# Optimization experiments

Measured on AMD Instinct MI355X. Metric: run time of the kernel, lower is better.

Reference implementation:

```python
import jax, jax.numpy as jnp
import numpy as np
from jax.scipy.special import logsumexp

# Complete binary tree, heap indexing: node i has children 2i+1, 2i+2.
# Edge for child c (c >= 1) is edge_pot[c-1], shape [C, C]:
#   rows = parent state, cols = child state (matches torch code's
#   logsumexp(edge + msg, dim=1) upward and edge.T downward).
DEPTH = 18
C = 16
N = 2 ** (DEPTH + 1) - 1  # 524287 nodes, N-1 edges


def setup_inputs() -> dict:
    key = jax.random.key(0)
    k1, k2 = jax.random.split(key)
    unary = jax.random.normal(k1, (N, C), dtype=jnp.float32)
    edge_pot = jax.random.normal(k2, (N - 1, C, C), dtype=jnp.float32)
    return {"unary": unary, "edge_pot": edge_pot, "depth": DEPTH}


def reference(unary, edge_pot, depth):
    """Sum-product belief propagation on a complete binary tree.

    Returns beliefs [N, C]: for each node v,
      belief[v] = unary[v] + sum(up messages from children) + down message from parent,
    identical to the per-message torch BFS loop, but processed level-parallel.
    """
    c = unary.shape[1]
    # ---------- upward pass (leaves -> root) ----------
    # subtotal[v] = unary[v] + sum of up-messages from v's children (V2F to parent factor)
    subtotal = unary
    m_up = jnp.zeros_like(unary)  # m_up[ch] = F2V message from edge (parent, ch) to parent
    for d in range(depth, 0, -1):
        lo, hi = 2 ** d - 1, 2 ** (d + 1) - 1          # children level, size 2^d
        ep = edge_pot[lo - 1:hi - 1]                    # [2^d, C, C]
        # logsumexp over child state (axis 2): torch's logsumexp(edge + msg, dim=1)
        msg = logsumexp(ep + subtotal[lo:hi][:, None, :], axis=2)  # [2^d, C]
        m_up = m_up.at[lo:hi].set(msg)
        plo, phi = 2 ** (d - 1) - 1, 2 ** d - 1
        # children of consecutive parents are consecutive pairs (2p+1, 2p+2)
        subtotal = subtotal.at[plo:phi].add(msg.reshape(-1, 2, c).sum(axis=1))
    # ---------- downward pass (root -> leaves) ----------
    m_down = jnp.zeros_like(unary)  # m_down[ch] = F2V message from edge (parent, ch) to ch
    for d in range(1, depth + 1):
        lo, hi = 2 ** d - 1, 2 ** (d + 1) - 1
        plo, phi = 2 ** (d - 1) - 1, 2 ** d - 1
        # V2F from parent p towards child ch: all incoming F2V at p except m_up[ch]
        par_total = jnp.repeat(subtotal[plo:phi] + m_down[plo:phi], 2, axis=0)  # [2^d, C]
        v2f = par_total - m_up[lo:hi]
        ep_t = jnp.swapaxes(edge_pot[lo - 1:hi - 1], 1, 2)  # edge.T: [2^d, Cchild, Cparent]
        msg = logsumexp(ep_t + v2f[:, None, :], axis=2)     # logsumexp over parent state
        m_down = m_down.at[lo:hi].set(msg)
    return subtotal + m_down  # beliefs [N, C]
```

## Files before the change

kernel.cpp:

```cpp
#include <hip/hip_runtime.h>
#include <stdint.h>


#ifndef __has_builtin
#define __has_builtin(x) 0
#endif
#if __has_builtin(__builtin_amdgcn_cvt_pk_fp8_f32) && __has_builtin(__builtin_amdgcn_cvt_f32_fp8)
#define EP8_FP8 1
#define EPC_BYTES 256
#else
#define EP8_FP8 0
#define EPC_BYTES 512
#endif

__device__ __forceinline__ void ldvec16(const float* p, float* d) {
    const float4* q = (const float4*)p;
    #pragma unroll
    for (int t = 0; t < 4; ++t) {
        float4 a = q[t];
        d[4*t+0] = a.x; d[4*t+1] = a.y; d[4*t+2] = a.z; d[4*t+3] = a.w;
    }
}

__device__ __forceinline__ float lse16_rs(const float* r, const float* s) {
    float v[16];
    float m;
    #pragma unroll
    for (int j = 0; j < 16; ++j) {
        v[j] = r[j] + s[j];
        m = (j == 0) ? v[0] : fmaxf(m, v[j]);
    }
    float acc = 0.f;
    #pragma unroll
    for (int j = 0; j < 16; ++j) acc += __expf(v[j] - m);
    return m + __logf(acc);
}

__device__ __forceinline__ void enc_row(uint8_t* dst, const float* r) {
#if EP8_FP8
    int w[4];
    #pragma unroll
    for (int t = 0; t < 4; ++t) {
        int x = __builtin_amdgcn_cvt_pk_fp8_f32(r[4*t+0], r[4*t+1], 0, false);
        x     = __builtin_amdgcn_cvt_pk_fp8_f32(r[4*t+2], r[4*t+3], x, true);
        w[t] = x;
    }
    *(int4*)dst = make_int4(w[0], w[1], w[2], w[3]);
#else
    uint32_t w[8];
    #pragma unroll
    for (int t = 0; t < 8; ++t) {
        uint32_t lo = __float_as_uint(r[2*t+0]);
        uint32_t hi = __float_as_uint(r[2*t+1]);
        w[t] = (lo >> 16) | (hi & 0xffff0000u);
    }
    ((int4*)dst)[0] = make_int4(w[0], w[1], w[2], w[3]);
    ((int4*)dst)[1] = make_int4(w[4], w[5], w[6], w[7]);
#endif
}

__device__ __forceinline__ void dec_row(const uint8_t* src, float* r) {
#if EP8_FP8
    uint4 w = *(const uint4*)src;
    uint32_t ws[4] = {w.x, w.y, w.z, w.w};
    #pragma unroll
    for (int t = 0; t < 4; ++t) {
        uint32_t u = ws[t];
        r[4*t+0] = __builtin_amdgcn_cvt_f32_fp8(u, 0);
        r[4*t+1] = __builtin_amdgcn_cvt_f32_fp8(u, 1);
        r[4*t+2] = __builtin_amdgcn_cvt_f32_fp8(u, 2);
        r[4*t+3] = __builtin_amdgcn_cvt_f32_fp8(u, 3);
    }
#else
    uint4 w0 = ((const uint4*)src)[0];
    uint4 w1 = ((const uint4*)src)[1];
    uint32_t ws[8] = {w0.x, w0.y, w0.z, w0.w, w1.x, w1.y, w1.z, w1.w};
    #pragma unroll
    for (int t = 0; t < 8; ++t) {
        r[2*t+0] = __uint_as_float(ws[t] << 16);
        r[2*t+1] = __uint_as_float(ws[t] & 0xffff0000u);
    }
#endif
}

__device__ __forceinline__ float dec_elem(const uint8_t* nodebase, int k, int i) {
#if EP8_FP8
    return __builtin_amdgcn_cvt_f32_fp8((uint32_t)nodebase[k*16 + i], 0);
#else
    uint32_t u = ((const uint16_t*)nodebase)[k*16 + i];
    return __uint_as_float(u << 16);
#endif
}

template <bool USE8>
__global__ __launch_bounds__(256) void up_sub(
    const float* __restrict__ unary, const float* __restrict__ ep,
    float* __restrict__ out, uint8_t* __restrict__ e8,
    int rl, int dl, int depth) {
    __shared__ float sub[2][32][16];
    int j = blockIdx.x;
    int cur = 0;
    for (int d = dl; d > rl; --d) {
        int np = 1 << (d - 1 - rl);
        size_t pbase = (((size_t)1 << (d - 1)) - 1) + (size_t)j * np;
        bool fromGlobal = (d == dl);
        const float* gsrc = (d == depth) ? unary : out;
        for (int t = threadIdx.x; t < np * 16; t += 256) {
            int pl = t >> 4, i = t & 15;
            size_t p = pbase + pl;
            size_t cl = 2 * p + 1, cr = cl + 1;
            float s[16], r[16];

            if (fromGlobal) ldvec16(gsrc + cl * 16, s);
            else            ldvec16(&sub[cur ^ 1][2 * pl][0], s);
            ldvec16(ep + (cl - 1) * 256 + i * 16, r);
            float msgL = lse16_rs(r, s);
            if (USE8) enc_row(e8 + (cl - 1) * EPC_BYTES + i * (EPC_BYTES / 16), r);

            if (fromGlobal) ldvec16(gsrc + cr * 16, s);
            else            ldvec16(&sub[cur ^ 1][2 * pl + 1][0], s);
            ldvec16(ep + (cr - 1) * 256 + i * 16, r);
            float msgR = lse16_rs(r, s);
            if (USE8) enc_row(e8 + (cr - 1) * EPC_BYTES + i * (EPC_BYTES / 16), r);

            float v = unary[p * 16 + i] + msgL + msgR;
            out[p * 16 + i] = v;
            if (d - 1 > rl) sub[cur][pl][i] = v;
        }
        __syncthreads();
        cur ^= 1;
    }
}

template <bool USE8>
__global__ __launch_bounds__(256) void down_sub(
    const float* __restrict__ unary, const float* __restrict__ ep,
    const uint8_t* __restrict__ e8, float* __restrict__ out,
    int rl, int dl, int depth) {
    __shared__ float bel[2][32][16];
    int j = blockIdx.x;
    int cur = 0;
    for (int d = rl + 1; d <= dl; ++d) {
        int nc = 1 << (d - rl);
        size_t cbase = (((size_t)1 << d) - 1) + (size_t)j * nc;
        bool leaf = (d == depth);
        bool parGlobal = (d == rl + 1);
        for (int t = threadIdx.x; t < nc * 16; t += 256) {
            int vl = t >> 4, i = t & 15;
            size_t v = cbase + vl;
            const float* ssrc = leaf ? unary : out;
            float s[16], r[16];
            ldvec16(ssrc + v * 16, s);
            float sub_i = ssrc[v * 16 + i];

            if (USE8) dec_row(e8 + (v - 1) * EPC_BYTES + i * (EPC_BYTES / 16), r);
            else      ldvec16(ep + (v - 1) * 256 + i * 16, r);
            float mup = lse16_rs(r, s);

            float pt;
            if (parGlobal) pt = out[((v - 1) >> 1) * 16 + i];
            else           pt = bel[cur ^ 1][vl >> 1][i];
            float v2f = pt - mup;

            float c[16];
            if (USE8) {
                const uint8_t* nb = e8 + (v - 1) * EPC_BYTES;
                #pragma unroll
                for (int k = 0; k < 16; ++k) c[k] = dec_elem(nb, k, i);
            } else {
                const float* nb = ep + (v - 1) * 256 + i;
                #pragma unroll
                for (int k = 0; k < 16; ++k) c[k] = nb[k * 16];
            }

            float vv[16], m;
            #pragma unroll
            for (int k = 0; k < 16; ++k) {
                float x = c[k] + __shfl(v2f, k, 16);
                vv[k] = x;
                m = (k == 0) ? x : fmaxf(m, x);
            }
            float acc = 0.f;
            #pragma unroll
            for (int k = 0; k < 16; ++k) acc += __expf(vv[k] - m);
            float msg = m + __logf(acc);

            float b = sub_i + msg;
            out[v * 16 + i] = b;
            if (d < dl) bel[cur][vl][i] = b;
        }
        __syncthreads();
        cur ^= 1;
    }
}

__device__ __forceinline__ void up_body_f32(const float* __restrict__ unary,
                                            const float* __restrict__ ep,
                                            float* out, size_t p, int i) {
    size_t cl = 2 * p + 1, cr = cl + 1;
    float s[16], r[16];
    ldvec16(out + cl * 16, s);
    ldvec16(ep + (cl - 1) * 256 + i * 16, r);
    float msgL = lse16_rs(r, s);
    ldvec16(out + cr * 16, s);
    ldvec16(ep + (cr - 1) * 256 + i * 16, r);
    float msgR = lse16_rs(r, s);
    out[p * 16 + i] = unary[p * 16 + i] + msgL + msgR;
}

__device__ __forceinline__ void down_body_f32(const float* __restrict__ ep,
                                              float* out, size_t v, int i) {
    size_t par = (v - 1) >> 1;
    float s[16], r[16];
    ldvec16(out + v * 16, s);
    float sub_i = out[v * 16 + i];
    ldvec16(ep + (v - 1) * 256 + i * 16, r);
    float mup = lse16_rs(r, s);
    float v2f = out[par * 16 + i] - mup;
    const float* nb = ep + (v - 1) * 256 + i;
    float c[16];
    #pragma unroll
    for (int k = 0; k < 16; ++k) c[k] = nb[k * 16];
    float vv[16], m;
    #pragma unroll
    for (int k = 0; k < 16; ++k) {
        float x = c[k] + __shfl(v2f, k, 16);
        vv[k] = x;
        m = (k == 0) ? x : fmaxf(m, x);
    }
    float acc = 0.f;
    #pragma unroll
    for (int k = 0; k < 16; ++k) acc += __expf(vv[k] - m);
    out[v * 16 + i] = sub_i + m + __logf(acc);
}

__global__ __launch_bounds__(1024) void top_fused(const float* __restrict__ unary,
                                                  const float* __restrict__ ep,
                                                  float* out, int FD) {
    int tid = threadIdx.x;
    for (int d = FD; d >= 1; --d) {
        int pcount = 1 << (d - 1);
        size_t plo = pcount - 1;
        for (int t = tid; t < pcount * 16; t += blockDim.x)
            up_body_f32(unary, ep, out, plo + (t >> 4), t & 15);
        __syncthreads();
    }
    for (int d = 1; d <= FD; ++d) {
        int count = 1 << d;
        size_t lo = count - 1;
        for (int t = tid; t < count * 16; t += blockDim.x)
            down_body_f32(ep, out, lo + (t >> 4), t & 15);
        __syncthreads();
    }
}

extern "C" void kernel_launch(void* const* d_in, const int* in_sizes, int n_in,
                              void* d_out, int out_size, void* d_ws, size_t ws_size,
                              hipStream_t stream) {
    const float* unary = (const float*)d_in[0];
    const float* ep    = (const float*)d_in[1];
    float* out = (float*)d_out;
    uint8_t* e8 = (uint8_t*)d_ws;

    int Nn = in_sizes[0] / 16;
    int depth = 0;
    while ((1 << (depth + 1)) < Nn + 1) ++depth;

    bool use8 = ws_size >= (size_t)(Nn - 1) * EPC_BYTES;

    int rls[8], dls[8], nch = 0;
    int dl = depth;
    if (depth > 6) {
        while (dl > 6) { rls[nch] = dl - 6; dls[nch] = dl; ++nch; dl -= 6; }
    } else {
        rls[0] = 0; dls[0] = depth; nch = 1; dl = 0;
    }
    int FD = dl;

    for (int c = 0; c < nch; ++c) {
        dim3 grid(1u << rls[c]), block(256);
        if (use8) up_sub<true ><<<grid, block, 0, stream>>>(unary, ep, out, e8, rls[c], dls[c], depth);
        else      up_sub<false><<<grid, block, 0, stream>>>(unary, ep, out, e8, rls[c], dls[c], depth);
    }
    if (FD > 0)
        top_fused<<<1, 1024, 0, stream>>>(unary, ep, out, FD);
    for (int c = nch - 1; c >= 0; --c) {
        dim3 grid(1u << rls[c]), block(256);
        if (use8) down_sub<true ><<<grid, block, 0, stream>>>(unary, ep, e8, out, rls[c], dls[c], depth);
        else      down_sub<false><<<grid, block, 0, stream>>>(unary, ep, e8, out, rls[c], dls[c], depth);
    }
}
```

Before: 268.5 us.

## Store exp-domain fp8 edge cache and bf16 up-messages; flat per-level kernels for deep levels

Deep levels (13..depth) now run as one flat kernel per level instead of the blocked subtree kernels. The upward pass caches exp(edge) in fp8 and stores each up-message in bf16. The downward pass then skips recomputing the up-message logsumexp, does a single exp per v2f element, and reduces the transposed product through shared memory. The aim is to cut the second full fp32 read of edge potentials and the redundant exp work on the down pass. The cost is more kernel launches and extra precision loss: exp of edge potentials in fp8 and messages in bf16 could breach tolerance. The fp8 path also no longer falls back to bf16 when the builtins are missing.

```diff
diff --git a/kernel.cpp b/kernel.cpp
--- a/kernel.cpp
+++ b/kernel.cpp
@@ -2,16 +2,7 @@
 #include <stdint.h>
 
 
-#ifndef __has_builtin
-#define __has_builtin(x) 0
-#endif
-#if __has_builtin(__builtin_amdgcn_cvt_pk_fp8_f32) && __has_builtin(__builtin_amdgcn_cvt_f32_fp8)
-#define EP8_FP8 1
-#define EPC_BYTES 256
-#else
-#define EP8_FP8 0
-#define EPC_BYTES 512
-#endif
+#define EPC 256
 
 __device__ __forceinline__ void ldvec16(const float* p, float* d) {
     const float4* q = (const float4*)p;
@@ -36,67 +27,156 @@
     return m + __logf(acc);
 }
 
-__device__ __forceinline__ void enc_row(uint8_t* dst, const float* r) {
-#if EP8_FP8
+__device__ __forceinline__ void enc_row(uint8_t* dst, const float* E) {
     int w[4];
     #pragma unroll
     for (int t = 0; t < 4; ++t) {
-        int x = __builtin_amdgcn_cvt_pk_fp8_f32(r[4*t+0], r[4*t+1], 0, false);
-        x     = __builtin_amdgcn_cvt_pk_fp8_f32(r[4*t+2], r[4*t+3], x, true);
+        int x = __builtin_amdgcn_cvt_pk_fp8_f32(E[4*t+0], E[4*t+1], 0, false);
+        x     = __builtin_amdgcn_cvt_pk_fp8_f32(E[4*t+2], E[4*t+3], x, true);
         w[t] = x;
     }
     *(int4*)dst = make_int4(w[0], w[1], w[2], w[3]);
-#else
-    uint32_t w[8];
-    #pragma unroll
-    for (int t = 0; t < 8; ++t) {
-        uint32_t lo = __float_as_uint(r[2*t+0]);
-        uint32_t hi = __float_as_uint(r[2*t+1]);
-        w[t] = (lo >> 16) | (hi & 0xffff0000u);
-    }
-    ((int4*)dst)[0] = make_int4(w[0], w[1], w[2], w[3]);
-    ((int4*)dst)[1] = make_int4(w[4], w[5], w[6], w[7]);
-#endif
-}
-
-__device__ __forceinline__ void dec_row(const uint8_t* src, float* r) {
-#if EP8_FP8
+}
+
+__device__ __forceinline__ void dec_row(const uint8_t* src, float* E) {
     uint4 w = *(const uint4*)src;
-    uint32_t ws[4] = {w.x, w.y, w.z, w.w};
-    #pragma unroll
-    for (int t = 0; t < 4; ++t) {
-        uint32_t u = ws[t];
-        r[4*t+0] = __builtin_amdgcn_cvt_f32_fp8(u, 0);
-        r[4*t+1] = __builtin_amdgcn_cvt_f32_fp8(u, 1);
-        r[4*t+2] = __builtin_amdgcn_cvt_f32_fp8(u, 2);
-        r[4*t+3] = __builtin_amdgcn_cvt_f32_fp8(u, 3);
-    }
-#else
-    uint4 w0 = ((const uint4*)src)[0];
-    uint4 w1 = ((const uint4*)src)[1];
-    uint32_t ws[8] = {w0.x, w0.y, w0.z, w0.w, w1.x, w1.y, w1.z, w1.w};
-    #pragma unroll
-    for (int t = 0; t < 8; ++t) {
-        r[2*t+0] = __uint_as_float(ws[t] << 16);
-        r[2*t+1] = __uint_as_float(ws[t] & 0xffff0000u);
-    }
-#endif
-}
-
-__device__ __forceinline__ float dec_elem(const uint8_t* nodebase, int k, int i) {
-#if EP8_FP8
-    return __builtin_amdgcn_cvt_f32_fp8((uint32_t)nodebase[k*16 + i], 0);
-#else
-    uint32_t u = ((const uint16_t*)nodebase)[k*16 + i];
-    return __uint_as_float(u << 16);
-#endif
+    uint32_t a;
+    a = w.x;
+    E[0]  = __builtin_amdgcn_cvt_f32_fp8(a, 0);
+    E[1]  = __builtin_amdgcn_cvt_f32_fp8(a, 1);
+    E[2]  = __builtin_amdgcn_cvt_f32_fp8(a, 2);
+    E[3]  = __builtin_amdgcn_cvt_f32_fp8(a, 3);
+    a = w.y;
+    E[4]  = __builtin_amdgcn_cvt_f32_fp8(a, 0);
+    E[5]  = __builtin_amdgcn_cvt_f32_fp8(a, 1);
+    E[6]  = __builtin_amdgcn_cvt_f32_fp8(a, 2);
+    E[7]  = __builtin_amdgcn_cvt_f32_fp8(a, 3);
+    a = w.z;
+    E[8]  = __builtin_amdgcn_cvt_f32_fp8(a, 0);
+    E[9]  = __builtin_amdgcn_cvt_f32_fp8(a, 1);
+    E[10] = __builtin_amdgcn_cvt_f32_fp8(a, 2);
+    E[11] = __builtin_amdgcn_cvt_f32_fp8(a, 3);
+    a = w.w;
+    E[12] = __builtin_amdgcn_cvt_f32_fp8(a, 0);
+    E[13] = __builtin_amdgcn_cvt_f32_fp8(a, 1);
+    E[14] = __builtin_amdgcn_cvt_f32_fp8(a, 2);
+    E[15] = __builtin_amdgcn_cvt_f32_fp8(a, 3);
+}
+
+__device__ __forceinline__ uint16_t f32_to_bf16(float x) {
+    uint32_t u = __float_as_uint(x);
+    u += 0x7fff + ((u >> 16) & 1);
+    return (uint16_t)(u >> 16);
+}
+__device__ __forceinline__ float bf16_to_f32(uint16_t h) {
+    return __uint_as_float((uint32_t)h << 16);
 }
 
 template <bool USE8>
-__global__ __launch_bounds__(256) void up_sub(
+__global__ __launch_bounds__(256) void up_flat(
+    const float* __restrict__ csrc, const float* __restrict__ unary,
+    const float* __restrict__ ep, float* __restrict__ out,
+    uint8_t* __restrict__ e8, uint16_t* __restrict__ mup,
+    int plo, int pcount) {
+    int t = blockIdx.x * 256 + threadIdx.x;
+    if (t >= pcount * 16) return;
+    int i = t & 15;
+    size_t p = (size_t)plo + (t >> 4);
+    size_t cl = 2 * p + 1;
+
+    float msg[2];
+    #pragma unroll
+    for (int ch = 0; ch < 2; ++ch) {
+        size_t c = cl + ch;
+        float s[16], r[16];
+        ldvec16(csrc + c * 16, s);
+        ldvec16(ep + (c - 1) * 256 + i * 16, r);
+        if (USE8) {
+            float E[16];
+            #pragma unroll
+            for (int j = 0; j < 16; ++j) E[j] = __expf(r[j]);
+            enc_row(e8 + (c - 1) * EPC + i * 16, E);
+            float m = s[0];
+            #pragma unroll
+            for (int j = 1; j < 16; ++j) m = fmaxf(m, s[j]);
+            float acc = 0.f;
+            #pragma unroll
+            for (int j = 0; j < 16; ++j) acc += E[j] * __expf(s[j] - m);
+            msg[ch] = __logf(acc) + m;
+            mup[c * 16 + i] = f32_to_bf16(msg[ch]);
+        } else {
+            msg[ch] = lse16_rs(r, s);
+        }
+    }
+    out[p * 16 + i] = unary[p * 16 + i] + msg[0] + msg[1];
+}
+
+template <bool USE8>
+__global__ __launch_bounds__(256) void down_flat(
+    const float* __restrict__ ssrc, const float* __restrict__ ep,
+    const uint8_t* __restrict__ e8, const uint16_t* __restrict__ mup,
+    float* __restrict__ out, int lo, int count) {
+    if (!USE8) {
+        int t = blockIdx.x * 256 + threadIdx.x;
+        if (t >= count * 16) return;
+        int i = t & 15;
+        size_t v = (size_t)lo + (t >> 4);
+        size_t par = (v - 1) >> 1;
+        float s[16], r[16];
+        ldvec16(ssrc + v * 16, s);
+        float sub_i = ssrc[v * 16 + i];
+        ldvec16(ep + (v - 1) * 256 + i * 16, r);
+        float mu = lse16_rs(r, s);
+        float v2f = out[par * 16 + i] - mu;
+        const float* nb = ep + (v - 1) * 256 + i;
+        float c[16];
+        #pragma unroll
+        for (int k = 0; k < 16; ++k) c[k] = nb[k * 16];
+        float vv[16], m;
+        #pragma unroll
+        for (int k = 0; k < 16; ++k) {
+            float x = c[k] + __shfl(v2f, k, 16);
+            vv[k] = x;
+            m = (k == 0) ? x : fmaxf(m, x);
+        }
+        float acc = 0.f;
+        #pragma unroll
+        for (int k = 0; k < 16; ++k) acc += __expf(vv[k] - m);
+        out[v * 16 + i] = sub_i + m + __logf(acc);
+        return;
+    }
+    __shared__ float T[16][16][20];
+    int g = threadIdx.x >> 4, i = threadIdx.x & 15;
+    size_t v = (size_t)lo + (size_t)(blockIdx.x * 16 + g);
+    size_t par = (v - 1) >> 1;
+
+    float sub_i = ssrc[v * 16 + i];
+    float pt    = out[par * 16 + i];
+    float mu    = bf16_to_f32(mup[v * 16 + i]);
+    float v2f   = pt - mu;
+
+    float m = v2f;
+    m = fmaxf(m, __shfl_xor(m, 1, 16));
+    m = fmaxf(m, __shfl_xor(m, 2, 16));
+    m = fmaxf(m, __shfl_xor(m, 4, 16));
+    m = fmaxf(m, __shfl_xor(m, 8, 16));
+    float u = __expf(v2f - m);
+
+    float E[16];
+    dec_row(e8 + (v - 1) * EPC + i * 16, E);
+    #pragma unroll
+    for (int j = 0; j < 16; ++j) T[g][i][j] = E[j] * u;
+    __syncthreads();
+    float acc = 0.f;
+    #pragma unroll
+    for (int k = 0; k < 16; ++k) acc += T[g][k][i];
+
+    out[v * 16 + i] = sub_i + __logf(acc) + m;
+}
+
+__global__ __launch_bounds__(256) void up_sub_f32(
     const float* __restrict__ unary, const float* __restrict__ ep,
-    float* __restrict__ out, uint8_t* __restrict__ e8,
-    int rl, int dl, int depth) {
+    float* __restrict__ out, int rl, int dl, int depth) {
     __shared__ float sub[2][32][16];
     int j = blockIdx.x;
     int cur = 0;
@@ -115,13 +195,11 @@
             else            ldvec16(&sub[cur ^ 1][2 * pl][0], s);
             ldvec16(ep + (cl - 1) * 256 + i * 16, r);
             float msgL = lse16_rs(r, s);
-            if (USE8) enc_row(e8 + (cl - 1) * EPC_BYTES + i * (EPC_BYTES / 16), r);
 
             if (fromGlobal) ldvec16(gsrc + cr * 16, s);
             else            ldvec16(&sub[cur ^ 1][2 * pl + 1][0], s);
             ldvec16(ep + (cr - 1) * 256 + i * 16, r);
             float msgR = lse16_rs(r, s);
-            if (USE8) enc_row(e8 + (cr - 1) * EPC_BYTES + i * (EPC_BYTES / 16), r);
 
             float v = unary[p * 16 + i] + msgL + msgR;
             out[p * 16 + i] = v;
@@ -132,11 +210,9 @@
     }
 }
 
-template <bool USE8>
-__global__ __launch_bounds__(256) void down_sub(
+__global__ __launch_bounds__(256) void down_sub_f32(
     const float* __restrict__ unary, const float* __restrict__ ep,
-    const uint8_t* __restrict__ e8, float* __restrict__ out,
-    int rl, int dl, int depth) {
+    float* __restrict__ out, int rl, int dl, int depth) {
     __shared__ float bel[2][32][16];
     int j = blockIdx.x;
     int cur = 0;
@@ -152,26 +228,18 @@
             float s[16], r[16];
             ldvec16(ssrc + v * 16, s);
             float sub_i = ssrc[v * 16 + i];
-
-            if (USE8) dec_row(e8 + (v - 1) * EPC_BYTES + i * (EPC_BYTES / 16), r);
-            else      ldvec16(ep + (v - 1) * 256 + i * 16, r);
-            float mup = lse16_rs(r, s);
+            ldvec16(ep + (v - 1) * 256 + i * 16, r);
+            float mu = lse16_rs(r, s);
 
             float pt;
             if (parGlobal) pt = out[((v - 1) >> 1) * 16 + i];
             else           pt = bel[cur ^ 1][vl >> 1][i];
-            float v2f = pt - mup;
-
+            float v2f = pt - mu;
+
+            const float* nb = ep + (v - 1) * 256 + i;
             float c[16];
-            if (USE8) {
-                const uint8_t* nb = e8 + (v - 1) * EPC_BYTES;
-                #pragma unroll
-                for (int k = 0; k < 16; ++k) c[k] = dec_elem(nb, k, i);
-            } else {
-                const float* nb = ep + (v - 1) * 256 + i;
-                #pragma unroll
-                for (int k = 0; k < 16; ++k) c[k] = nb[k * 16];
-            }
+            #pragma unroll
+            for (int k = 0; k < 16; ++k) c[k] = nb[k * 16];
 
             float vv[16], m;
             #pragma unroll
@@ -183,9 +251,7 @@
             float acc = 0.f;
             #pragma unroll
             for (int k = 0; k < 16; ++k) acc += __expf(vv[k] - m);
-            float msg = m + __logf(acc);
-
-            float b = sub_i + msg;
+            float b = sub_i + m + __logf(acc);
             out[v * 16 + i] = b;
             if (d < dl) bel[cur][vl][i] = b;
         }
@@ -215,8 +281,8 @@
     ldvec16(out + v * 16, s);
     float sub_i = out[v * 16 + i];
     ldvec16(ep + (v - 1) * 256 + i * 16, r);
-    float mup = lse16_rs(r, s);
-    float v2f = out[par * 16 + i] - mup;
+    float mu = lse16_rs(r, s);
+    float v2f = out[par * 16 + i] - mu;
     const float* nb = ep + (v - 1) * 256 + i;
     float c[16];
     #pragma unroll
@@ -260,33 +326,55 @@
     const float* unary = (const float*)d_in[0];
     const float* ep    = (const float*)d_in[1];
     float* out = (float*)d_out;
-    uint8_t* e8 = (uint8_t*)d_ws;
 
     int Nn = in_sizes[0] / 16;
     int depth = 0;
     while ((1 << (depth + 1)) < Nn + 1) ++depth;
 
-    bool use8 = ws_size >= (size_t)(Nn - 1) * EPC_BYTES;
-
-    int rls[8], dls[8], nch = 0;
-    int dl = depth;
-    if (depth > 6) {
-        while (dl > 6) { rls[nch] = dl - 6; dls[nch] = dl; ++nch; dl -= 6; }
+    uint8_t* e8 = (uint8_t*)d_ws;
+    size_t e8_bytes = (size_t)Nn * EPC;
+    size_t mup_off = (e8_bytes + 255) & ~(size_t)255;
+    uint16_t* mup = (uint16_t*)((uint8_t*)d_ws + mup_off);
+    size_t need = mup_off + (size_t)Nn * 16 * 2;
+    bool use8 = ws_size >= need;
+
+    if (use8 && depth >= 13) {
+        for (int d = depth; d >= 13; --d) {
+            int pcount = 1 << (d - 1);
+            int plo = pcount - 1;
+            const float* csrc = (d == depth) ? unary : out;
+            up_flat<true><<<pcount * 16 / 256, 256, 0, stream>>>(
+                csrc, unary, ep, out, e8, mup, plo, pcount);
+        }
+        up_sub_f32<<<64, 256, 0, stream>>>(unary, ep, out, 6, 12, depth);
+        top_fused<<<1, 1024, 0, stream>>>(unary, ep, out, 6);
+        down_sub_f32<<<64, 256, 0, stream>>>(unary, ep, out, 6, 12, depth);
+        for (int d = 13; d <= depth; ++d) {
+            int count = 1 << d;
+            int lo = count - 1;
+            const float* ssrc = (d == depth) ? unary : out;
+            down_flat<true><<<count * 16 / 256, 256, 0, stream>>>(
+                ssrc, ep, e8, mup, out, lo, count);
+        }
     } else {
-        rls[0] = 0; dls[0] = depth; nch = 1; dl = 0;
-    }
-    int FD = dl;
-
-    for (int c = 0; c < nch; ++c) {
-        dim3 grid(1u << rls[c]), block(256);
-        if (use8) up_sub<true ><<<grid, block, 0, stream>>>(unary, ep, out, e8, rls[c], dls[c], depth);
-        else      up_sub<false><<<grid, block, 0, stream>>>(unary, ep, out, e8, rls[c], dls[c], depth);
-    }
-    if (FD > 0)
-        top_fused<<<1, 1024, 0, stream>>>(unary, ep, out, FD);
-    for (int c = nch - 1; c >= 0; --c) {
-        dim3 grid(1u << rls[c]), block(256);
-        if (use8) down_sub<true ><<<grid, block, 0, stream>>>(unary, ep, e8, out, rls[c], dls[c], depth);
-        else      down_sub<false><<<grid, block, 0, stream>>>(unary, ep, e8, out, rls[c], dls[c], depth);
-    }
-}
+        int FD = (depth >= 2) ? ((depth - 1 < 6) ? depth - 1 : 6) : 0;
+        for (int d = depth; d > FD; --d) {
+            int pcount = 1 << (d - 1);
+            int plo = pcount - 1;
+            const float* csrc = (d == depth) ? unary : out;
+            dim3 grid((pcount * 16 + 255) / 256);
+            up_flat<false><<<grid, 256, 0, stream>>>(
+                csrc, unary, ep, out, e8, mup, plo, pcount);
+        }
+        if (FD > 0)
+            top_fused<<<1, 1024, 0, stream>>>(unary, ep, out, FD);
+        for (int d = FD + 1; d <= depth; ++d) {
+            int count = 1 << d;
+            int lo = count - 1;
+            const float* ssrc = (d == depth) ? unary : out;
+            dim3 grid((count * 16 + 255) / 256);
+            down_flat<false><<<grid, 256, 0, stream>>>(
+                ssrc, ep, e8, mup, out, lo, count);
+        }
+    }
+}
```

New measurement: 249.9 us. 6.9% less time.
